# Performance work log

Measured on AMD Instinct MI355X. Metric: run time of the kernel, lower is better.

Reference implementation:

```python
import jax, jax.numpy as jnp
import numpy as np

N = 20000   # nodes
E = 320000  # edges (before self loops)
IN = 128    # in_channel
H = 8       # heads
C = 128     # out_channels per head
HC = H * C  # 1024
G = 64      # graphs in batch


def _w(k, shape):
    s = 1.0 / np.sqrt(shape[-1])
    return jax.random.uniform(k, shape, jnp.float32, -s, s)


def setup_inputs() -> dict:
    key = jax.random.key(0)
    ks = jax.random.split(key, 12)
    return {
        "x": jax.random.normal(ks[0], (N, IN), jnp.float32),
        "edge_index": jax.random.randint(ks[1], (2, E), 0, N, dtype=jnp.int64),
        "batch": jnp.sort(jax.random.randint(ks[2], (N,), 0, G, dtype=jnp.int64)),
        # GATv2Conv params
        "Wl": _w(ks[3], (HC, IN)), "bl": jnp.zeros((HC,), jnp.float32),
        "Wr": _w(ks[4], (HC, IN)), "br": jnp.zeros((HC,), jnp.float32),
        "att": _w(ks[5], (H, C)),
        "Wres": _w(ks[6], (HC, IN)),
        "bias_conv": jnp.zeros((HC,), jnp.float32),
        # post-attention Linear(HC -> C)
        "Wlin": _w(ks[7], (C, HC)), "blin": jnp.zeros((C,), jnp.float32),
        # MLP head 128 -> 16 -> 32 -> 5
        "W1": _w(ks[8], (16, C)), "b1": jnp.zeros((16,), jnp.float32),
        "W2": _w(ks[9], (32, 16)), "b2": jnp.zeros((32,), jnp.float32),
        "W3": _w(ks[10], (5, 32)), "b3": jnp.zeros((5,), jnp.float32),
    }


def reference(x, edge_index, batch, Wl, bl, Wr, br, att, Wres, bias_conv,
              Wlin, blin, W1, b1, W2, b2, W3, b3):
    # --- GATv2Conv (PyG semantics: add_self_loops=True, concat=True, residual) ---
    loops = jnp.arange(N)
    src = jnp.concatenate([edge_index[0], loops])  # [E+N]
    dst = jnp.concatenate([edge_index[1], loops])
    x_l = (x @ Wl.T + bl).reshape(N, H, C)
    x_r = (x @ Wr.T + br).reshape(N, H, C)
    # per-edge attention logits
    e = jax.nn.leaky_relu(x_l[src] + x_r[dst], 0.2)        # [E+N, H, C]
    logits = jnp.einsum('ehc,hc->eh', e, att)              # [E+N, H]
    # segment softmax over destination neighborhoods
    m = jax.ops.segment_max(logits, dst, num_segments=N)
    a = jnp.exp(logits - m[dst])
    denom = jax.ops.segment_sum(a, dst, num_segments=N)
    alpha = a / (denom[dst] + 1e-16)                       # [E+N, H]
    # scatter-add weighted messages
    out = jax.ops.segment_sum(x_l[src] * alpha[:, :, None], dst,
                              num_segments=N).reshape(N, HC)
    out = out + x @ Wres.T + bias_conv                     # residual + bias
    # --- Linear + ELU ---
    h = jax.nn.elu(out @ Wlin.T + blin)                    # [N, C]
    # --- global mean pool per graph ---
    cnt = jax.ops.segment_sum(jnp.ones((N,), h.dtype), batch, num_segments=G)
    pooled = jax.ops.segment_sum(h, batch, num_segments=G) / jnp.maximum(cnt, 1.0)[:, None]
    # --- MLP head ---
    y = jax.nn.relu(pooled @ W1.T + b1)
    y = jax.nn.relu(y @ W2.T + b2)
    return y @ W3.T + b3                                   # [G, 5]
```

## Files before the change

### kernel.cpp

```cpp
#include <hip/hip_runtime.h>
#include <hip/hip_bf16.h>
#include <math.h>

#define N_NODES 20000
#define N_EDGES 320000
#define IN_CH   128
#define HEADS   8
#define CPH     128
#define HCH     1024
#define NG      64
#define ETOT    (N_EDGES + N_NODES)
#define NCVT    768

typedef __attribute__((ext_vector_type(8))) short s8v;
typedef __attribute__((ext_vector_type(4))) float f4v;
typedef __attribute__((ext_vector_type(8))) float f8v;
typedef __attribute__((ext_vector_type(4))) unsigned short u16x4;
typedef __attribute__((ext_vector_type(8))) unsigned short u16x8;

__device__ __forceinline__ unsigned short bf16_rne(float f) {
    unsigned u = __float_as_uint(f);
    unsigned r = u + 0x7fffu + ((u >> 16) & 1u);
    return (unsigned short)(r >> 16);
}
__device__ __forceinline__ float bf16_to_f(unsigned short h) {
    return __uint_as_float((unsigned)h << 16);
}

__global__ void init_kernel(int* __restrict__ deg, float* __restrict__ pooled) {
    int i = blockIdx.x * blockDim.x + threadIdx.x;
    if (i < N_NODES) deg[i] = 0;
    if (i < NG * CPH) pooled[i] = 0.0f;
}

__global__ void cvt_all(const float* __restrict__ x,  const float* __restrict__ Wl,
                        const float* __restrict__ Wr, const float* __restrict__ Wlin,
                        unsigned short* __restrict__ xhi,  unsigned short* __restrict__ xlo,
                        unsigned short* __restrict__ wlhi, unsigned short* __restrict__ wllo,
                        unsigned short* __restrict__ wrhi, unsigned short* __restrict__ wrlo,
                        unsigned short* __restrict__ wnhi, unsigned short* __restrict__ wnlo,
                        const int* __restrict__ ei, int* __restrict__ deg,
                        const float* __restrict__ Wres, const float* __restrict__ bias_conv,
                        const float* __restrict__ blin,
                        unsigned short* __restrict__ wchi, unsigned short* __restrict__ wclo,
                        float* __restrict__ bcomb)
{
    const int t = threadIdx.x;
    if (blockIdx.x < NCVT) {
        const int NX = N_NODES * IN_CH, NW = HCH * IN_CH;
        const int TOT4 = (NX + 3 * NW) >> 2;
        const int stride = NCVT * 256;
        for (int q = blockIdx.x * 256 + t; q < TOT4; q += stride) {
            int i = q << 2;
            const float* s; unsigned short *hi, *lo; int k;
            if (i < NX)               { s = x;    hi = xhi;  lo = xlo;  k = i; }
            else if (i < NX + NW)     { s = Wl;   hi = wlhi; lo = wllo; k = i - NX; }
            else if (i < NX + 2 * NW) { s = Wr;   hi = wrhi; lo = wrlo; k = i - NX - NW; }
            else                      { s = Wlin; hi = wnhi; lo = wnlo; k = i - NX - 2 * NW; }
            f4v f = *(const f4v*)&s[k];
            u16x4 h, l;
            #pragma unroll
            for (int e = 0; e < 4; ++e) {
                unsigned short hh = bf16_rne(f[e]);
                h[e] = hh;
                l[e] = bf16_rne(f[e] - bf16_to_f(hh));
            }
            *(u16x4*)&hi[k] = h;
            *(u16x4*)&lo[k] = l;
        }
        for (int e = blockIdx.x * 256 + t; e < ETOT; e += stride) {
            int dst = (e < N_EDGES) ? ei[N_EDGES + e] : (e - N_EDGES);
            atomicAdd(&deg[dst], 1);
        }
    } else if (t < 128) {
        const int j = blockIdx.x - NCVT;
        float s = 0.0f, pb = 0.0f;
        for (int m = 0; m < HCH; ++m) {
            float wl = Wlin[j * HCH + m];
            s  += wl * Wres[m * IN_CH + t];
            pb += wl * bias_conv[m];
        }
        unsigned short h = bf16_rne(s);
        wchi[j * IN_CH + t] = h;
        wclo[j * IN_CH + t] = bf16_rne(s - bf16_to_f(h));
        if (t == 0) bcomb[j] = blin[j] + pb;
    }
}

__global__ __launch_bounds__(256) void proj_gemm(
    const unsigned short* __restrict__ Ahi, const unsigned short* __restrict__ Alo,
    const unsigned short* __restrict__ WLhi, const unsigned short* __restrict__ WLlo,
    const unsigned short* __restrict__ WRhi, const unsigned short* __restrict__ WRlo,
    const float* __restrict__ bl, const float* __restrict__ br,
    const float* __restrict__ att,
    unsigned short* __restrict__ xl_h, unsigned short* __restrict__ xr_h,
    float* __restrict__ dl, float* __restrict__ dr, int M)
{
    __shared__ unsigned short cst[128][136];
    const int t    = threadIdx.x;
    const int wave = t >> 6, lane = t & 63;
    const int wr = wave >> 1, wc = wave & 1;
    const int l15 = lane & 15, lg = lane >> 4;
    const int m0 = blockIdx.x * 128 + wr * 64;
    const int by = blockIdx.y;
    const int sel = by >> 3;
    const int hh  = by & 7;
    const int col0 = hh * 128;
    const unsigned short* Whi = sel ? WRhi : WLhi;
    const unsigned short* Wlo = sel ? WRlo : WLlo;
    const float* bias = sel ? br : bl;
    unsigned short* C = sel ? xr_h : xl_h;
    float* D = sel ? dr : dl;
    const int koff = lg * 8;
    const int K = IN_CH;

    int rowA[4], colB[4];
    #pragma unroll
    for (int i = 0; i < 4; ++i) { int r = m0 + i * 16 + l15; rowA[i] = r < M ? r : M - 1; }
    #pragma unroll
    for (int j = 0; j < 4; ++j) colB[j] = col0 + wc * 64 + j * 16 + l15;

    float bj[4];
    #pragma unroll
    for (int j = 0; j < 4; ++j) bj[j] = bias[colB[j]];

    f4v acc[4][4];
    #pragma unroll
    for (int i = 0; i < 4; ++i)
        #pragma unroll
        for (int j = 0; j < 4; ++j) acc[i][j] = (f4v){0.f, 0.f, 0.f, 0.f};

    for (int k0 = 0; k0 < K; k0 += 32) {
        s8v ah[4], al[4], bh[4], blv[4];
        #pragma unroll
        for (int i = 0; i < 4; ++i) {
            size_t off = (size_t)rowA[i] * K + k0 + koff;
            ah[i] = *(const s8v*)&Ahi[off];
            al[i] = *(const s8v*)&Alo[off];
        }
        #pragma unroll
        for (int j = 0; j < 4; ++j) {
            size_t off = (size_t)colB[j] * K + k0 + koff;
            bh[j]  = *(const s8v*)&Whi[off];
            blv[j] = *(const s8v*)&Wlo[off];
        }
        #pragma unroll
        for (int i = 0; i < 4; ++i)
            #pragma unroll
            for (int j = 0; j < 4; ++j) {
                acc[i][j] = __builtin_amdgcn_mfma_f32_16x16x32_bf16(ah[i], bh[j],  acc[i][j], 0, 0, 0);
                acc[i][j] = __builtin_amdgcn_mfma_f32_16x16x32_bf16(ah[i], blv[j], acc[i][j], 0, 0, 0);
                acc[i][j] = __builtin_amdgcn_mfma_f32_16x16x32_bf16(al[i], bh[j],  acc[i][j], 0, 0, 0);
            }
    }

    #pragma unroll
    for (int i = 0; i < 4; ++i)
        #pragma unroll
        for (int r = 0; r < 4; ++r) {
            int lr = wr * 64 + i * 16 + lg * 4 + r;
            #pragma unroll
            for (int j = 0; j < 4; ++j)
                cst[lr][wc * 64 + j * 16 + l15] = bf16_rne(acc[i][j][r] + bj[j]);
        }
    __syncthreads();

    {
        const int c8  = (t & 15) * 8;
        const int r16 = t >> 4;
        #pragma unroll
        for (int it = 0; it < 8; ++it) {
            int lr = it * 16 + r16;
            int row = blockIdx.x * 128 + lr;
            if (row >= M) continue;
            u16x8 v = *(const u16x8*)&cst[lr][c8];
            *(u16x8*)&C[(size_t)row * HCH + col0 + c8] = v;
        }
    }

    {
        const int r2  = t >> 1;
        const int ch0 = (t & 1) * 64;
        float q = 0.0f;
        #pragma unroll
        for (int c = 0; c < 64; c += 8) {
            u16x8 cv = *(const u16x8*)&cst[r2][ch0 + c];
            f4v a0 = *(const f4v*)&att[hh * 128 + ch0 + c];
            f4v a1 = *(const f4v*)&att[hh * 128 + ch0 + c + 4];
            q = fmaf(a0[0], bf16_to_f(cv[0]), q);
            q = fmaf(a0[1], bf16_to_f(cv[1]), q);
            q = fmaf(a0[2], bf16_to_f(cv[2]), q);
            q = fmaf(a0[3], bf16_to_f(cv[3]), q);
            q = fmaf(a1[0], bf16_to_f(cv[4]), q);
            q = fmaf(a1[1], bf16_to_f(cv[5]), q);
            q = fmaf(a1[2], bf16_to_f(cv[6]), q);
            q = fmaf(a1[3], bf16_to_f(cv[7]), q);
        }
        q += __shfl_xor(q, 1, 64);
        int row = blockIdx.x * 128 + r2;
        if ((t & 1) == 0 && row < M) D[row * 8 + hh] = q;
    }
}

__global__ __launch_bounds__(128) void mfma_gemm2(
    const unsigned short* __restrict__ A1h,
    const unsigned short* __restrict__ B1hi, const unsigned short* __restrict__ B1lo, int K1,
    const unsigned short* __restrict__ A2hi, const unsigned short* __restrict__ A2lo,
    const unsigned short* __restrict__ B2hi, const unsigned short* __restrict__ B2lo, int K2,
    const float* __restrict__ bias, const int* __restrict__ batch,
    float* __restrict__ pooled, int M)
{
    __shared__ float cst[64][130];
    __shared__ int batch_s[64];
    const int t    = threadIdx.x;
    const int wc   = t >> 6, lane = t & 63;
    const int l15 = lane & 15, lg = lane >> 4;
    const int m0 = blockIdx.x * 64;
    const int n0 = wc * 64;
    const int koff = lg * 8;

    if (t < 64) {
        int row = m0 + t;
        batch_s[t] = (row < M) ? batch[row] : -1;
    }

    int rowA[4], colB[4];
    #pragma unroll
    for (int i = 0; i < 4; ++i) { int r = m0 + i * 16 + l15; rowA[i] = r < M ? r : M - 1; }
    #pragma unroll
    for (int j = 0; j < 4; ++j) colB[j] = n0 + j * 16 + l15;

    float bj[4];
    #pragma unroll
    for (int j = 0; j < 4; ++j) bj[j] = bias[colB[j]];

    f4v acc[4][4];
    #pragma unroll
    for (int i = 0; i < 4; ++i)
        #pragma unroll
        for (int j = 0; j < 4; ++j) acc[i][j] = (f4v){0.f, 0.f, 0.f, 0.f};

    for (int k0 = 0; k0 < K1; k0 += 32) {
        s8v ah[4], bh[4], blv[4];
        #pragma unroll
        for (int i = 0; i < 4; ++i)
            ah[i] = *(const s8v*)&A1h[(size_t)rowA[i] * K1 + k0 + koff];
        #pragma unroll
        for (int j = 0; j < 4; ++j) {
            size_t off = (size_t)colB[j] * K1 + k0 + koff;
            bh[j]  = *(const s8v*)&B1hi[off];
            blv[j] = *(const s8v*)&B1lo[off];
        }
        #pragma unroll
        for (int i = 0; i < 4; ++i)
            #pragma unroll
            for (int j = 0; j < 4; ++j) {
                acc[i][j] = __builtin_amdgcn_mfma_f32_16x16x32_bf16(ah[i], bh[j],  acc[i][j], 0, 0, 0);
                acc[i][j] = __builtin_amdgcn_mfma_f32_16x16x32_bf16(ah[i], blv[j], acc[i][j], 0, 0, 0);
            }
    }
    for (int k0 = 0; k0 < K2; k0 += 32) {
        s8v ah[4], al[4], bh[4], blv[4];
        #pragma unroll
        for (int i = 0; i < 4; ++i) {
            size_t off = (size_t)rowA[i] * K2 + k0 + koff;
            ah[i] = *(const s8v*)&A2hi[off];
            al[i] = *(const s8v*)&A2lo[off];
        }
        #pragma unroll
        for (int j = 0; j < 4; ++j) {
            size_t off = (size_t)colB[j] * K2 + k0 + koff;
            bh[j]  = *(const s8v*)&B2hi[off];
            blv[j] = *(const s8v*)&B2lo[off];
        }
        #pragma unroll
        for (int i = 0; i < 4; ++i)
            #pragma unroll
            for (int j = 0; j < 4; ++j) {
                acc[i][j] = __builtin_amdgcn_mfma_f32_16x16x32_bf16(ah[i], bh[j],  acc[i][j], 0, 0, 0);
                acc[i][j] = __builtin_amdgcn_mfma_f32_16x16x32_bf16(ah[i], blv[j], acc[i][j], 0, 0, 0);
                acc[i][j] = __builtin_amdgcn_mfma_f32_16x16x32_bf16(al[i], bh[j],  acc[i][j], 0, 0, 0);
            }
    }

    #pragma unroll
    for (int i = 0; i < 4; ++i)
        #pragma unroll
        for (int r = 0; r < 4; ++r) {
            int lr = i * 16 + lg * 4 + r;
            #pragma unroll
            for (int j = 0; j < 4; ++j) {
                float v = acc[i][j][r] + bj[j];
                v = v > 0.0f ? v : expm1f(v);
                cst[lr][n0 + j * 16 + l15] = v;
            }
        }
    __syncthreads();

    const int col = t;
    float run = 0.0f;
    int cur_g = -2;
    #pragma unroll 4
    for (int r = 0; r < 64; ++r) {
        int g = batch_s[r];
        if (g != cur_g) {
            if (cur_g >= 0) atomicAdd(&pooled[cur_g * CPH + col], run);
            run = 0.0f; cur_g = g;
        }
        if (g >= 0) run += cst[r][col];
    }
    if (cur_g >= 0) atomicAdd(&pooled[cur_g * CPH + col], run);
}

__global__ __launch_bounds__(256) void scan_kernel(
    const int* __restrict__ deg, int* __restrict__ rowptr, int* __restrict__ wof)
{
    __shared__ int wsum[4];
    __shared__ int carry_s;
    const int t = threadIdx.x, wave = t >> 6, lane = t & 63;
    if (t == 0) { carry_s = 0; rowptr[0] = 0; }
    __syncthreads();
    for (int base = 0; base < N_NODES; base += 1024) {
        int idx = base + t * 4;
        int d[4], p[4];
        #pragma unroll
        for (int k = 0; k < 4; ++k)
            d[k] = (idx + k < N_NODES) ? deg[idx + k] : 0;
        p[0] = d[0]; p[1] = p[0] + d[1]; p[2] = p[1] + d[2]; p[3] = p[2] + d[3];
        int v = p[3];
        #pragma unroll
        for (int off = 1; off < 64; off <<= 1) {
            int u = __shfl_up(v, off, 64);
            if (lane >= off) v += u;
        }
        if (lane == 63) wsum[wave] = v;
        __syncthreads();
        int woff = carry_s;
        #pragma unroll
        for (int w = 0; w < 4; ++w) if (w < wave) woff += wsum[w];
        int tbase = woff + v - p[3];
        #pragma unroll
        for (int k = 0; k < 4; ++k) {
            if (idx + k < N_NODES) {
                rowptr[idx + k + 1] = tbase + p[k];
                wof[idx + k] = tbase + p[k] - d[k];
            }
        }
        __syncthreads();
        if (t == 255) carry_s = woff + v;
        __syncthreads();
    }
}

__global__ void scatter_kernel(const int* __restrict__ ei, int* __restrict__ wof,
                               int* __restrict__ csr_src)
{
    for (int e = blockIdx.x * blockDim.x + threadIdx.x; e < ETOT;
         e += gridDim.x * blockDim.x) {
        int src, dst;
        if (e < N_EDGES) { src = ei[e]; dst = ei[N_EDGES + e]; }
        else             { src = dst = e - N_EDGES; }
        int p = atomicAdd(&wof[dst], 1);
        csr_src[p] = src;
    }
}

__global__ __launch_bounds__(128) void agg_fused(
    const unsigned short* __restrict__ xl_h, const unsigned short* __restrict__ xr_h,
    const float* __restrict__ att,
    const float* __restrict__ dl, const float* __restrict__ dr,
    const int* __restrict__ rowptr, const int* __restrict__ csr_src,
    unsigned short* __restrict__ agg_h)
{
    const int dst = blockIdx.x;
    const int t = threadIdx.x;
    const int h = t >> 4;
    const int beg = rowptr[dst], end = rowptr[dst + 1];

    const u16x8 bh8 = *(const u16x8*)&xr_h[(size_t)dst * HCH + t * 8];
    f8v b;
    #pragma unroll
    for (int e = 0; e < 8; ++e) b[e] = bf16_to_f(bh8[e]);
    f8v w04;
    {
        f4v a0 = *(const f4v*)&att[t * 8];
        f4v a1 = *(const f4v*)&att[t * 8 + 4];
        #pragma unroll
        for (int e = 0; e < 4; ++e) { w04[e] = 0.4f * a0[e]; w04[e + 4] = 0.4f * a1[e]; }
    }
    const float pb = 0.6f * dr[dst * 8 + h];

    float m = -__builtin_inff(), s = 0.0f;
    f8v acc = {0.f, 0.f, 0.f, 0.f, 0.f, 0.f, 0.f, 0.f};

    int j = beg;
    for (; j + 1 < end; j += 2) {
        const int s0 = csr_src[j], s1 = csr_src[j + 1];
        const u16x8 vh0 = *(const u16x8*)&xl_h[(size_t)s0 * HCH + t * 8];
        const u16x8 vh1 = *(const u16x8*)&xl_h[(size_t)s1 * HCH + t * 8];
        const float d0 = dl[s0 * 8 + h], d1 = dl[s1 * 8 + h];
        f8v v0, v1;
        #pragma unroll
        for (int e = 0; e < 8; ++e) { v0[e] = bf16_to_f(vh0[e]); v1[e] = bf16_to_f(vh1[e]); }

        float q0 = w04[0] * __builtin_fabsf(v0[0] + b[0]);
        float q1 = w04[0] * __builtin_fabsf(v1[0] + b[0]);
        #pragma unroll
        for (int e = 1; e < 8; ++e) {
            q0 = fmaf(w04[e], __builtin_fabsf(v0[e] + b[e]), q0);
            q1 = fmaf(w04[e], __builtin_fabsf(v1[e] + b[e]), q1);
        }
        #pragma unroll
        for (int off = 8; off; off >>= 1) {
            q0 += __shfl_xor(q0, off, 16);
            q1 += __shfl_xor(q1, off, 16);
        }
        const float p0 = fmaf(0.6f, d0, q0) + pb;
        const float p1 = fmaf(0.6f, d1, q1) + pb;

        const float mx = fmaxf(p0, p1);
        if (mx > m) {
            float scale = __expf(m - mx);
            float e0 = __expf(p0 - mx), e1 = __expf(p1 - mx);
            s = s * scale + e0 + e1;
            acc = acc * scale + v0 * e0 + v1 * e1;
            m = mx;
        } else {
            float e0 = __expf(p0 - m), e1 = __expf(p1 - m);
            s += e0 + e1;
            acc += v0 * e0 + v1 * e1;
        }
    }
    if (j < end) {
        const int s0 = csr_src[j];
        const u16x8 vh0 = *(const u16x8*)&xl_h[(size_t)s0 * HCH + t * 8];
        const float d0 = dl[s0 * 8 + h];
        f8v v0;
        #pragma unroll
        for (int e = 0; e < 8; ++e) v0[e] = bf16_to_f(vh0[e]);
        float q0 = w04[0] * __builtin_fabsf(v0[0] + b[0]);
        #pragma unroll
        for (int e = 1; e < 8; ++e)
            q0 = fmaf(w04[e], __builtin_fabsf(v0[e] + b[e]), q0);
        #pragma unroll
        for (int off = 8; off; off >>= 1) q0 += __shfl_xor(q0, off, 16);
        const float p0 = fmaf(0.6f, d0, q0) + pb;
        if (p0 > m) {
            float scale = __expf(m - p0);
            s = s * scale + 1.0f;
            acc = acc * scale + v0;
            m = p0;
        } else {
            float e0 = __expf(p0 - m);
            s += e0;
            acc += v0 * e0;
        }
    }

    const float inv = 1.0f / (s + 1e-16f);
    f8v r = acc * inv;
    u16x8 hv;
    #pragma unroll
    for (int e = 0; e < 8; ++e) hv[e] = bf16_rne(r[e]);
    *(u16x8*)&agg_h[(size_t)dst * HCH + t * 8] = hv;
}

__global__ __launch_bounds__(64) void head_kernel(
    const float* __restrict__ pooled, const int* __restrict__ batch,
    const float* __restrict__ W1, const float* __restrict__ b1,
    const float* __restrict__ W2, const float* __restrict__ b2,
    const float* __restrict__ W3, const float* __restrict__ b3,
    float* __restrict__ out)
{
    const int g = threadIdx.x;
    int lo = 0, hi = N_NODES;
    while (lo < hi) { int mid = (lo + hi) >> 1; if (batch[mid] <  g) lo = mid + 1; else hi = mid; }
    const int s0 = lo;
    hi = N_NODES;
    while (lo < hi) { int mid = (lo + hi) >> 1; if (batch[mid] <= g) lo = mid + 1; else hi = mid; }
    const float inv = 1.0f / fmaxf((float)(lo - s0), 1.0f);

    float y1[16];
    for (int j = 0; j < 16; ++j) {
        float s = b1[j];
        for (int k = 0; k < CPH; ++k) s += W1[j * CPH + k] * (pooled[g * CPH + k] * inv);
        y1[j] = fmaxf(s, 0.0f);
    }
    float y2[32];
    for (int j = 0; j < 32; ++j) {
        float s = b2[j];
        for (int k = 0; k < 16; ++k) s += W2[j * 16 + k] * y1[k];
        y2[j] = fmaxf(s, 0.0f);
    }
    for (int u = 0; u < 5; ++u) {
        float s = b3[u];
        for (int k = 0; k < 32; ++k) s += W3[u * 32 + k] * y2[k];
        out[g * 5 + u] = s;
    }
}

extern "C" void kernel_launch(void* const* d_in, const int* in_sizes, int n_in,
                              void* d_out, int out_size, void* d_ws, size_t ws_size,
                              hipStream_t stream)
{
    const float* x         = (const float*)d_in[0];
    const int*   ei        = (const int*)  d_in[1];
    const int*   batch     = (const int*)  d_in[2];
    const float* Wl        = (const float*)d_in[3];
    const float* bl        = (const float*)d_in[4];
    const float* Wr        = (const float*)d_in[5];
    const float* br        = (const float*)d_in[6];
    const float* att       = (const float*)d_in[7];
    const float* Wres      = (const float*)d_in[8];
    const float* bias_conv = (const float*)d_in[9];
    const float* Wlin      = (const float*)d_in[10];
    const float* blin      = (const float*)d_in[11];
    const float* W1        = (const float*)d_in[12];
    const float* b1        = (const float*)d_in[13];
    const float* W2        = (const float*)d_in[14];
    const float* b2        = (const float*)d_in[15];
    const float* W3        = (const float*)d_in[16];
    const float* b3        = (const float*)d_in[17];
    float* out = (float*)d_out;

    unsigned short* xl_h  = (unsigned short*)d_ws;
    unsigned short* xr_h  = xl_h + (size_t)N_NODES * HCH;
    unsigned short* agg_h = xr_h + (size_t)N_NODES * HCH;
    float* pooled = (float*)(agg_h + (size_t)N_NODES * HCH);
    float* bcomb  = pooled + NG * CPH;
    float* dl     = bcomb + 128;
    float* dr     = dl + (size_t)N_NODES * 8;
    unsigned short* x_hi  = (unsigned short*)(dr + (size_t)N_NODES * 8);
    unsigned short* x_lo  = x_hi  + (size_t)N_NODES * IN_CH;
    unsigned short* wl_hi = x_lo  + (size_t)N_NODES * IN_CH;
    unsigned short* wl_lo = wl_hi + HCH * IN_CH;
    unsigned short* wr_hi = wl_lo + HCH * IN_CH;
    unsigned short* wr_lo = wr_hi + HCH * IN_CH;
    unsigned short* wn_hi = wr_lo + HCH * IN_CH;
    unsigned short* wn_lo = wn_hi + CPH * HCH;
    unsigned short* wc_hi = wn_lo + CPH * HCH;
    unsigned short* wc_lo = wc_hi + CPH * IN_CH;
    int* deg     = (int*)(wc_lo + CPH * IN_CH);
    int* rowptr  = deg + N_NODES;
    int* wof     = rowptr + N_NODES + 1;
    int* csr_src = wof + N_NODES;

    init_kernel<<<(N_NODES + 255) / 256, 256, 0, stream>>>(deg, pooled);

    cvt_all<<<NCVT + 128, 256, 0, stream>>>(x, Wl, Wr, Wlin,
                                            x_hi, x_lo, wl_hi, wl_lo,
                                            wr_hi, wr_lo, wn_hi, wn_lo,
                                            ei, deg,
                                            Wres, bias_conv, blin,
                                            wc_hi, wc_lo, bcomb);

    dim3 gp((N_NODES + 127) / 128, 16);
    proj_gemm<<<gp, 256, 0, stream>>>(x_hi, x_lo, wl_hi, wl_lo, wr_hi, wr_lo,
                                      bl, br, att, xl_h, xr_h, dl, dr, N_NODES);

    scan_kernel<<<1, 256, 0, stream>>>(deg, rowptr, wof);
    scatter_kernel<<<1024, 256, 0, stream>>>(ei, wof, csr_src);

    agg_fused<<<N_NODES, 128, 0, stream>>>(xl_h, xr_h, att, dl, dr,
                                           rowptr, csr_src, agg_h);

    dim3 g2((N_NODES + 63) / 64, 1);
    mfma_gemm2<<<g2, 128, 0, stream>>>(agg_h, wn_hi, wn_lo, HCH,
                                       x_hi, x_lo, wc_hi, wc_lo, IN_CH,
                                       bcomb, batch, pooled, N_NODES);

    head_kernel<<<1, 64, 0, stream>>>(pooled, batch, W1, b1, W2, b2, W3, b3, out);
}
```

Baseline: 426.7 us.

## Split each destination's edge list across two thread groups with LDS softmax merge

The aggregation kernel now uses 256 threads per destination node, in two 128-thread groups. Each group handles alternating pairs of incoming edges and keeps its own online-softmax state. The partial max, sum and accumulators are merged through shared memory before the output is written. This aims to double the edge-level parallelism and memory-level parallelism per node. In exchange it adds LDS traffic, a block barrier and one idle group during the final merge. The launch is also split into two half-grid launches, which adds launch overhead.

```diff
diff --git a/kernel.cpp b/kernel.cpp
--- a/kernel.cpp
+++ b/kernel.cpp
@@ -365,26 +365,30 @@
     }
 }
 
-__global__ __launch_bounds__(128) void agg_fused(
+__global__ __launch_bounds__(256) void agg_fused(
     const unsigned short* __restrict__ xl_h, const unsigned short* __restrict__ xr_h,
     const float* __restrict__ att,
     const float* __restrict__ dl, const float* __restrict__ dr,
     const int* __restrict__ rowptr, const int* __restrict__ csr_src,
-    unsigned short* __restrict__ agg_h)
-{
-    const int dst = blockIdx.x;
+    unsigned short* __restrict__ agg_h, int dst0)
+{
+    __shared__ float lds_m[128], lds_s[128];
+    __shared__ float lds_acc[8][128];
+    const int dst = blockIdx.x + dst0;
     const int t = threadIdx.x;
-    const int h = t >> 4;
+    const int grp = t >> 7;
+    const int u = t & 127;
+    const int h = u >> 4;
     const int beg = rowptr[dst], end = rowptr[dst + 1];
 
-    const u16x8 bh8 = *(const u16x8*)&xr_h[(size_t)dst * HCH + t * 8];
+    const u16x8 bh8 = *(const u16x8*)&xr_h[(size_t)dst * HCH + u * 8];
     f8v b;
     #pragma unroll
     for (int e = 0; e < 8; ++e) b[e] = bf16_to_f(bh8[e]);
     f8v w04;
     {
-        f4v a0 = *(const f4v*)&att[t * 8];
-        f4v a1 = *(const f4v*)&att[t * 8 + 4];
+        f4v a0 = *(const f4v*)&att[u * 8];
+        f4v a1 = *(const f4v*)&att[u * 8 + 4];
         #pragma unroll
         for (int e = 0; e < 4; ++e) { w04[e] = 0.4f * a0[e]; w04[e + 4] = 0.4f * a1[e]; }
     }
@@ -393,11 +397,11 @@
     float m = -__builtin_inff(), s = 0.0f;
     f8v acc = {0.f, 0.f, 0.f, 0.f, 0.f, 0.f, 0.f, 0.f};
 
-    int j = beg;
-    for (; j + 1 < end; j += 2) {
+    int j = beg + grp * 2;
+    for (; j + 1 < end; j += 4) {
         const int s0 = csr_src[j], s1 = csr_src[j + 1];
-        const u16x8 vh0 = *(const u16x8*)&xl_h[(size_t)s0 * HCH + t * 8];
-        const u16x8 vh1 = *(const u16x8*)&xl_h[(size_t)s1 * HCH + t * 8];
+        const u16x8 vh0 = *(const u16x8*)&xl_h[(size_t)s0 * HCH + u * 8];
+        const u16x8 vh1 = *(const u16x8*)&xl_h[(size_t)s1 * HCH + u * 8];
         const float d0 = dl[s0 * 8 + h], d1 = dl[s1 * 8 + h];
         f8v v0, v1;
         #pragma unroll
@@ -433,7 +437,7 @@
     }
     if (j < end) {
         const int s0 = csr_src[j];
-        const u16x8 vh0 = *(const u16x8*)&xl_h[(size_t)s0 * HCH + t * 8];
+        const u16x8 vh0 = *(const u16x8*)&xl_h[(size_t)s0 * HCH + u * 8];
         const float d0 = dl[s0 * 8 + h];
         f8v v0;
         #pragma unroll
@@ -457,12 +461,28 @@
         }
     }
 
-    const float inv = 1.0f / (s + 1e-16f);
-    f8v r = acc * inv;
-    u16x8 hv;
-    #pragma unroll
-    for (int e = 0; e < 8; ++e) hv[e] = bf16_rne(r[e]);
-    *(u16x8*)&agg_h[(size_t)dst * HCH + t * 8] = hv;
+    if (grp == 1) {
+        lds_m[u] = m;
+        lds_s[u] = s;
+        #pragma unroll
+        for (int e = 0; e < 8; ++e) lds_acc[e][u] = acc[e];
+    }
+    __syncthreads();
+    if (grp == 0) {
+        const float m1 = lds_m[u], s1 = lds_s[u];
+        const float M  = fmaxf(m, m1);
+        const float c0 = __expf(m - M);
+        const float c1 = __expf(m1 - M);
+        const float S  = s * c0 + s1 * c1;
+        const float inv = 1.0f / (S + 1e-16f);
+        u16x8 hv;
+        #pragma unroll
+        for (int e = 0; e < 8; ++e) {
+            float r = (acc[e] * c0 + lds_acc[e][u] * c1) * inv;
+            hv[e] = bf16_rne(r);
+        }
+        *(u16x8*)&agg_h[(size_t)dst * HCH + u * 8] = hv;
+    }
 }
 
 __global__ __launch_bounds__(64) void head_kernel(
@@ -561,8 +581,10 @@
     scan_kernel<<<1, 256, 0, stream>>>(deg, rowptr, wof);
     scatter_kernel<<<1024, 256, 0, stream>>>(ei, wof, csr_src);
 
-    agg_fused<<<N_NODES, 128, 0, stream>>>(xl_h, xr_h, att, dl, dr,
-                                           rowptr, csr_src, agg_h);
+    agg_fused<<<N_NODES / 2, 256, 0, stream>>>(xl_h, xr_h, att, dl, dr,
+                                               rowptr, csr_src, agg_h, 0);
+    agg_fused<<<N_NODES / 2, 256, 0, stream>>>(xl_h, xr_h, att, dl, dr,
+                                               rowptr, csr_src, agg_h, N_NODES / 2);
 
     dim3 g2((N_NODES + 63) / 64, 1);
     mfma_gemm2<<<g2, 128, 0, stream>>>(agg_h, wn_hi, wn_lo, HCH,
```

Result: no change. 432.7 us (+1.4%).
